# Kernel tuning notes

Measured on AMD Instinct MI355X. Metric: run time of the kernel, lower is better.

## Reference

```python
import jax, jax.numpy as jnp
import numpy as np
from jax import lax

KERNEL = 3
SAMPLING_RATE = 100.0
N_GRID = 201  # np.linspace(-1, 1, 201) sub-sample grid


def setup_inputs() -> dict:
    key = jax.random.key(0)
    nb, nc, nx, nt = 32, 3, 64, 4096
    xcorr = jax.random.normal(key, (nb, nc, nx, nt), dtype=jnp.float32)
    return {"xcorr": xcorr, "nlag": nt // 2}


def reference(xcorr, nlag):
    nt = xcorr.shape[-1]
    x = jnp.abs(xcorr)  # vabs=True

    # max_pool2d with (1, kernel=3), stride 1, padding (0, 1) -> SAME max over lag axis
    smax = lax.reduce_window(
        x, -jnp.inf, lax.max,
        window_dimensions=(1, 1, 1, KERNEL),
        window_strides=(1, 1, 1, 1),
        padding=[(0, 0), (0, 0), (0, 0), (KERNEL // 2, KERNEL // 2)],
    )
    keep = (smax == x).astype(x.dtype)

    # top-2 local maxima along lag axis (sorted descending, like torch.topk)
    topk_score, topk_idx = lax.top_k(x * keep, 2)
    s0 = topk_score[..., 0]
    s1 = topk_score[..., 1]
    weight = (0.1 + 3.0 * (s0 - s1)) * s0 ** 2
    i0 = topk_idx[..., 0]  # [nb, nc, nx]

    # --- sub-sample interpolation: 3-point spline == parabola through neighbors ---
    offsets = jnp.array([-1, 0, 1], dtype=i0.dtype)
    nbr_idx = jnp.clip(i0[..., None] + offsets, 0, nt - 1)      # [nb,nc,nx,3]
    y = jnp.take_along_axis(x, nbr_idx, axis=-1)                 # [nb,nc,nx,3]
    ym1, y0, yp1 = y[..., 0], y[..., 1], y[..., 2]
    a = 0.5 * (ym1 + yp1) - y0   # quadratic coeff
    b = 0.5 * (yp1 - ym1)        # linear coeff
    c = y0                       # constant

    xg = jnp.linspace(-1.0, 1.0, N_GRID, dtype=x.dtype)          # [201]
    yg = (a[..., None] * xg + b[..., None]) * xg + c[..., None]  # [nb,nc,nx,201]
    ii = jnp.argmax(yg, axis=-1)                                  # [nb,nc,nx]
    sub_shift = xg[ii]
    topk_idx_f = i0.astype(x.dtype) + sub_shift
    topk_score0 = jnp.take_along_axis(yg, ii[..., None], axis=-1)[..., 0]

    # pick the channel with the largest weight
    idx = jnp.argmax(weight, axis=1, keepdims=True)               # [nb,1,nx]
    max_cc = jnp.take_along_axis(topk_score0, idx, axis=1)
    w = jnp.take_along_axis(weight, idx, axis=1)
    shift_idx = jnp.take_along_axis(topk_idx_f, idx, axis=1) - jnp.asarray(nlag, x.dtype)
    shift_t = shift_idx / SAMPLING_RATE

    # stacked: [cc_max, cc_weight, cc_dt, cc_shift], each [nb,1,nx]
    return jnp.stack([max_cc, w, shift_t, shift_idx], axis=0)
```

## Files before the change

### kernel.cpp

```cpp
#include <hip/hip_runtime.h>
#include <math.h>

#define NB 32
#define NC 3
#define NX 64
#define NT 4096
#define NGRID 201

__device__ __forceinline__ bool better(float va, int ia, float vb, int ib) {
    return (va > vb) || (va == vb && ia < ib);
}

__global__ __launch_bounds__(256) void detect_peaks_kernel(
    const float* __restrict__ xcorr,
    const int*   __restrict__ nlag_p,
    float* __restrict__ out)
{
    __shared__ float rv0[4], rv1[4];
    __shared__ int   ri0[4], ri1[4];

    const int bid  = blockIdx.x;
    const int b    = bid / NX;
    const int x    = bid % NX;
    const int tid  = threadIdx.x;
    const int lane = tid & 63;
    const int wid  = tid >> 6;

    float best_w = -INFINITY, best_s = 0.0f, best_f = 0.0f;

    for (int c = 0; c < NC; ++c) {
        const float* __restrict__ xr =
            xcorr + ((size_t)((b * NC + c) * NX) + x) * NT;

        float v0 = -1.0f, v1 = -1.0f;
        int   i0 = 0x7fffffff, i1 = 0x7fffffff;

        #pragma unroll
        for (int k = 0; k < 4; ++k) {
            const int t4 = (k * 256 + tid) * 4;
            const float4 v = *reinterpret_cast<const float4*>(xr + t4);
            const float a0 = fabsf(v.x), a1 = fabsf(v.y);
            const float a2 = fabsf(v.z), a3 = fabsf(v.w);

            float lm = __shfl_up(a3, 1);
            float rm = __shfl_down(a0, 1);
            if (lane == 0)  lm = (t4 > 0)      ? fabsf(xr[t4 - 1]) : -INFINITY;
            if (lane == 63) rm = (t4 + 4 < NT) ? fabsf(xr[t4 + 4]) : -INFINITY;

            const float c0 = (a0 >= lm && a0 >= a1) ? a0 : 0.0f;
            const float c1 = (a1 >= a0 && a1 >= a2) ? a1 : 0.0f;
            const float c2 = (a2 >= a1 && a2 >= a3) ? a2 : 0.0f;
            const float c3 = (a3 >= a2 && a3 >= rm) ? a3 : 0.0f;

            if (c0 > v0)      { v1 = v0; i1 = i0; v0 = c0; i0 = t4;     }
            else if (c0 > v1) { v1 = c0; i1 = t4;                       }
            if (c1 > v0)      { v1 = v0; i1 = i0; v0 = c1; i0 = t4 + 1; }
            else if (c1 > v1) { v1 = c1; i1 = t4 + 1;                   }
            if (c2 > v0)      { v1 = v0; i1 = i0; v0 = c2; i0 = t4 + 2; }
            else if (c2 > v1) { v1 = c2; i1 = t4 + 2;                   }
            if (c3 > v0)      { v1 = v0; i1 = i0; v0 = c3; i0 = t4 + 3; }
            else if (c3 > v1) { v1 = c3; i1 = t4 + 3;                   }
        }

        #pragma unroll
        for (int off = 1; off < 64; off <<= 1) {
            const float ov0 = __shfl_xor(v0, off);
            const int   oi0 = __shfl_xor(i0, off);
            const float ov1 = __shfl_xor(v1, off);
            const int   oi1 = __shfl_xor(i1, off);
            if (better(ov0, oi0, v0, i0)) {
                float nv1; int ni1;
                if (better(v0, i0, ov1, oi1)) { nv1 = v0;  ni1 = i0;  }
                else                          { nv1 = ov1; ni1 = oi1; }
                v0 = ov0; i0 = oi0; v1 = nv1; i1 = ni1;
            } else {
                if (better(ov0, oi0, v1, i1)) { v1 = ov0; i1 = oi0; }
            }
        }

        if (lane == 0) { rv0[wid] = v0; ri0[wid] = i0; rv1[wid] = v1; ri1[wid] = i1; }
        __syncthreads();

        if (tid < 64) {
            float a0 = rv0[0], a1 = rv1[0];
            int   ai0 = ri0[0], ai1 = ri1[0];
            #pragma unroll
            for (int w = 1; w < 4; ++w) {
                const float b0 = rv0[w], b1 = rv1[w];
                const int   bi0 = ri0[w], bi1 = ri1[w];
                if (better(b0, bi0, a0, ai0)) {
                    float nv1; int ni1;
                    if (better(a0, ai0, b1, bi1)) { nv1 = a0; ni1 = ai0; }
                    else                          { nv1 = b1; ni1 = bi1; }
                    a0 = b0; ai0 = bi0; a1 = nv1; ai1 = ni1;
                } else {
                    if (better(b0, bi0, a1, ai1)) { a1 = b0; ai1 = bi0; }
                }
            }

            const float s0 = a0, s1 = a1;
            const int   p0 = ai0;
            const float weight = (0.1f + 3.0f * (s0 - s1)) * (s0 * s0);

            const int im1 = (p0 - 1 < 0) ? 0 : p0 - 1;
            const int ip1 = (p0 + 1 > NT - 1) ? NT - 1 : p0 + 1;
            const float ym1 = fabsf(xr[im1]);
            const float yc  = fabsf(xr[p0]);
            const float yp1 = fabsf(xr[ip1]);
            const float A = 0.5f * (ym1 + yp1) - yc;
            const float B = 0.5f * (yp1 - ym1);
            const float C = yc;

            float bv = -INFINITY; int bi = 0x7fffffff;
            #pragma unroll
            for (int k = 0; k < 4; ++k) {
                const int gi = lane + k * 64;
                if (gi < NGRID) {
                    const float xg = 0.01f * (float)(gi - 100);
                    const float yg = (A * xg + B) * xg + C;
                    if (yg > bv) { bv = yg; bi = gi; }
                }
            }
            #pragma unroll
            for (int off = 1; off < 64; off <<= 1) {
                const float ov = __shfl_xor(bv, off);
                const int   oi = __shfl_xor(bi, off);
                if (ov > bv || (ov == bv && oi < bi)) { bv = ov; bi = oi; }
            }

            if (weight > best_w) {
                best_w = weight;
                best_s = bv;
                best_f = (float)p0 + 0.01f * (float)(bi - 100);
            }
        }
        __syncthreads();
    }

    if (tid == 0) {
        const float nlagf = (float)(*nlag_p);
        const int n = NB * NX;
        const int o = b * NX + x;
        const float shift_idx = best_f - nlagf;
        out[0 * n + o] = best_s;
        out[1 * n + o] = best_w;
        out[2 * n + o] = shift_idx / 100.0f;
        out[3 * n + o] = shift_idx;
    }
}

extern "C" void kernel_launch(void* const* d_in, const int* in_sizes, int n_in,
                              void* d_out, int out_size, void* d_ws, size_t ws_size,
                              hipStream_t stream) {
    const float* xcorr  = (const float*)d_in[0];
    const int*   nlag_p = (const int*)d_in[1];
    float* out = (float*)d_out;

    detect_peaks_kernel<<<NB * NX, 256, 0, stream>>>(xcorr, nlag_p, out);
}
```

Baseline: 29.26 us.

## Process all channels in one pass and carry peak neighbors through reductions

```diff
diff --git a/kernel.cpp b/kernel.cpp
--- a/kernel.cpp
+++ b/kernel.cpp
@@ -16,8 +16,8 @@
     const int*   __restrict__ nlag_p,
     float* __restrict__ out)
 {
-    __shared__ float rv0[4], rv1[4];
-    __shared__ int   ri0[4], ri1[4];
+    __shared__ float sv0[NC][4], sv1[NC][4], snm[NC][4], snp[NC][4];
+    __shared__ int   si0[NC][4], si1[NC][4];
 
     const int bid  = blockIdx.x;
     const int b    = bid / NX;
@@ -26,90 +26,112 @@
     const int lane = tid & 63;
     const int wid  = tid >> 6;
 
-    float best_w = -INFINITY, best_s = 0.0f, best_f = 0.0f;
+    const float* __restrict__ xr0 =
+        xcorr + ((size_t)(b * NC) * NX + x) * NT;
 
+    float v0[NC], v1[NC], n0m[NC], n0p[NC];
+    int   i0[NC], i1[NC];
+    #pragma unroll
     for (int c = 0; c < NC; ++c) {
-        const float* __restrict__ xr =
-            xcorr + ((size_t)((b * NC + c) * NX) + x) * NT;
+        v0[c] = -1.0f; v1[c] = -1.0f;
+        i0[c] = 0x7fffffff; i1[c] = 0x7fffffff;
+        n0m[c] = 0.0f; n0p[c] = 0.0f;
+    }
 
-        float v0 = -1.0f, v1 = -1.0f;
-        int   i0 = 0x7fffffff, i1 = 0x7fffffff;
-
+    #pragma unroll
+    for (int k = 0; k < 4; ++k) {
+        const int t4 = (k * 256 + tid) * 4;
         #pragma unroll
-        for (int k = 0; k < 4; ++k) {
-            const int t4 = (k * 256 + tid) * 4;
+        for (int c = 0; c < NC; ++c) {
+            const float* __restrict__ xr = xr0 + (size_t)c * (NX * NT);
             const float4 v = *reinterpret_cast<const float4*>(xr + t4);
             const float a0 = fabsf(v.x), a1 = fabsf(v.y);
             const float a2 = fabsf(v.z), a3 = fabsf(v.w);
 
             float lm = __shfl_up(a3, 1);
             float rm = __shfl_down(a0, 1);
-            if (lane == 0)  lm = (t4 > 0)      ? fabsf(xr[t4 - 1]) : -INFINITY;
-            if (lane == 63) rm = (t4 + 4 < NT) ? fabsf(xr[t4 + 4]) : -INFINITY;
+            if (lane == 0 && t4 > 0)        lm = fabsf(xr[t4 - 1]);
+            if (lane == 63 && t4 + 4 < NT)  rm = fabsf(xr[t4 + 4]);
+            const bool has_l = (t4 > 0);
+            const bool has_r = (t4 + 4 < NT);
+            const float cmp_l = has_l ? lm : -INFINITY;
+            const float cmp_r = has_r ? rm : -INFINITY;
+            const float par_l = has_l ? lm : a0;
+            const float par_r = has_r ? rm : a3;
 
-            const float c0 = (a0 >= lm && a0 >= a1) ? a0 : 0.0f;
+            const float c0 = (a0 >= cmp_l && a0 >= a1) ? a0 : 0.0f;
             const float c1 = (a1 >= a0 && a1 >= a2) ? a1 : 0.0f;
             const float c2 = (a2 >= a1 && a2 >= a3) ? a2 : 0.0f;
-            const float c3 = (a3 >= a2 && a3 >= rm) ? a3 : 0.0f;
+            const float c3 = (a3 >= a2 && a3 >= cmp_r) ? a3 : 0.0f;
 
-            if (c0 > v0)      { v1 = v0; i1 = i0; v0 = c0; i0 = t4;     }
-            else if (c0 > v1) { v1 = c0; i1 = t4;                       }
-            if (c1 > v0)      { v1 = v0; i1 = i0; v0 = c1; i0 = t4 + 1; }
-            else if (c1 > v1) { v1 = c1; i1 = t4 + 1;                   }
-            if (c2 > v0)      { v1 = v0; i1 = i0; v0 = c2; i0 = t4 + 2; }
-            else if (c2 > v1) { v1 = c2; i1 = t4 + 2;                   }
-            if (c3 > v0)      { v1 = v0; i1 = i0; v0 = c3; i0 = t4 + 3; }
-            else if (c3 > v1) { v1 = c3; i1 = t4 + 3;                   }
+            if (c0 > v0[c])      { v1[c]=v0[c]; i1[c]=i0[c]; v0[c]=c0; i0[c]=t4;   n0m[c]=par_l; n0p[c]=a1; }
+            else if (c0 > v1[c]) { v1[c]=c0; i1[c]=t4; }
+            if (c1 > v0[c])      { v1[c]=v0[c]; i1[c]=i0[c]; v0[c]=c1; i0[c]=t4+1; n0m[c]=a0; n0p[c]=a2; }
+            else if (c1 > v1[c]) { v1[c]=c1; i1[c]=t4+1; }
+            if (c2 > v0[c])      { v1[c]=v0[c]; i1[c]=i0[c]; v0[c]=c2; i0[c]=t4+2; n0m[c]=a1; n0p[c]=a3; }
+            else if (c2 > v1[c]) { v1[c]=c2; i1[c]=t4+2; }
+            if (c3 > v0[c])      { v1[c]=v0[c]; i1[c]=i0[c]; v0[c]=c3; i0[c]=t4+3; n0m[c]=a2; n0p[c]=par_r; }
+            else if (c3 > v1[c]) { v1[c]=c3; i1[c]=t4+3; }
         }
+    }
+
+    #pragma unroll
+    for (int c = 0; c < NC; ++c) {
+        #pragma unroll
+        for (int off = 1; off < 64; off <<= 1) {
+            const float ov0 = __shfl_xor(v0[c], off);
+            const int   oi0 = __shfl_xor(i0[c], off);
+            const float ov1 = __shfl_xor(v1[c], off);
+            const int   oi1 = __shfl_xor(i1[c], off);
+            const float onm = __shfl_xor(n0m[c], off);
+            const float onp = __shfl_xor(n0p[c], off);
+            if (better(ov0, oi0, v0[c], i0[c])) {
+                float nv1; int ni1;
+                if (better(v0[c], i0[c], ov1, oi1)) { nv1 = v0[c]; ni1 = i0[c]; }
+                else                                { nv1 = ov1;   ni1 = oi1;   }
+                v0[c] = ov0; i0[c] = oi0; n0m[c] = onm; n0p[c] = onp;
+                v1[c] = nv1; i1[c] = ni1;
+            } else {
+                if (better(ov0, oi0, v1[c], i1[c])) { v1[c] = ov0; i1[c] = oi0; }
+            }
+        }
+        if (lane == 0) {
+            sv0[c][wid] = v0[c]; si0[c][wid] = i0[c];
+            sv1[c][wid] = v1[c]; si1[c][wid] = i1[c];
+            snm[c][wid] = n0m[c]; snp[c][wid] = n0p[c];
+        }
+    }
+    __syncthreads();
+
+    if (tid < 64) {
+        float best_w = -INFINITY, best_s = 0.0f, best_f = 0.0f;
 
         #pragma unroll
-        for (int off = 1; off < 64; off <<= 1) {
-            const float ov0 = __shfl_xor(v0, off);
-            const int   oi0 = __shfl_xor(i0, off);
-            const float ov1 = __shfl_xor(v1, off);
-            const int   oi1 = __shfl_xor(i1, off);
-            if (better(ov0, oi0, v0, i0)) {
-                float nv1; int ni1;
-                if (better(v0, i0, ov1, oi1)) { nv1 = v0;  ni1 = i0;  }
-                else                          { nv1 = ov1; ni1 = oi1; }
-                v0 = ov0; i0 = oi0; v1 = nv1; i1 = ni1;
-            } else {
-                if (better(ov0, oi0, v1, i1)) { v1 = ov0; i1 = oi0; }
-            }
-        }
-
-        if (lane == 0) { rv0[wid] = v0; ri0[wid] = i0; rv1[wid] = v1; ri1[wid] = i1; }
-        __syncthreads();
-
-        if (tid < 64) {
-            float a0 = rv0[0], a1 = rv1[0];
-            int   ai0 = ri0[0], ai1 = ri1[0];
+        for (int c = 0; c < NC; ++c) {
+            float m0 = sv0[c][0], m1 = sv1[c][0];
+            int  mi0 = si0[c][0], mi1 = si1[c][0];
+            float nm = snm[c][0], np = snp[c][0];
             #pragma unroll
             for (int w = 1; w < 4; ++w) {
-                const float b0 = rv0[w], b1 = rv1[w];
-                const int   bi0 = ri0[w], bi1 = ri1[w];
-                if (better(b0, bi0, a0, ai0)) {
+                const float b0 = sv0[c][w], b1 = sv1[c][w];
+                const int  bi0 = si0[c][w], bi1 = si1[c][w];
+                if (better(b0, bi0, m0, mi0)) {
                     float nv1; int ni1;
-                    if (better(a0, ai0, b1, bi1)) { nv1 = a0; ni1 = ai0; }
+                    if (better(m0, mi0, b1, bi1)) { nv1 = m0; ni1 = mi0; }
                     else                          { nv1 = b1; ni1 = bi1; }
-                    a0 = b0; ai0 = bi0; a1 = nv1; ai1 = ni1;
+                    m0 = b0; mi0 = bi0; nm = snm[c][w]; np = snp[c][w];
+                    m1 = nv1; mi1 = ni1;
                 } else {
-                    if (better(b0, bi0, a1, ai1)) { a1 = b0; ai1 = bi0; }
+                    if (better(b0, bi0, m1, mi1)) { m1 = b0; mi1 = bi0; }
                 }
             }
 
-            const float s0 = a0, s1 = a1;
-            const int   p0 = ai0;
+            const float s0 = m0, s1 = m1;
             const float weight = (0.1f + 3.0f * (s0 - s1)) * (s0 * s0);
 
-            const int im1 = (p0 - 1 < 0) ? 0 : p0 - 1;
-            const int ip1 = (p0 + 1 > NT - 1) ? NT - 1 : p0 + 1;
-            const float ym1 = fabsf(xr[im1]);
-            const float yc  = fabsf(xr[p0]);
-            const float yp1 = fabsf(xr[ip1]);
-            const float A = 0.5f * (ym1 + yp1) - yc;
-            const float B = 0.5f * (yp1 - ym1);
-            const float C = yc;
+            const float A = 0.5f * (nm + np) - s0;
+            const float B = 0.5f * (np - nm);
+            const float C = s0;
 
             float bv = -INFINITY; int bi = 0x7fffffff;
             #pragma unroll
@@ -131,21 +153,20 @@
             if (weight > best_w) {
                 best_w = weight;
                 best_s = bv;
-                best_f = (float)p0 + 0.01f * (float)(bi - 100);
+                best_f = (float)mi0 + 0.01f * (float)(bi - 100);
             }
         }
-        __syncthreads();
-    }
 
-    if (tid == 0) {
-        const float nlagf = (float)(*nlag_p);
-        const int n = NB * NX;
-        const int o = b * NX + x;
-        const float shift_idx = best_f - nlagf;
-        out[0 * n + o] = best_s;
-        out[1 * n + o] = best_w;
-        out[2 * n + o] = shift_idx / 100.0f;
-        out[3 * n + o] = shift_idx;
+        if (lane == 0) {
+            const float nlagf = (float)(*nlag_p);
+            const int n = NB * NX;
+            const int o = b * NX + x;
+            const float shift_idx = best_f - nlagf;
+            out[0 * n + o] = best_s;
+            out[1 * n + o] = best_w;
+            out[2 * n + o] = shift_idx / 100.0f;
+            out[3 * n + o] = shift_idx;
+        }
     }
 }
 
```

Measured after the change: 46.14 us. 57.7% more time.

## Prefetch all three channel rows and compute sub-sample peak analytically

Applied to the files above, without the earlier changes.

```diff
diff --git a/kernel.cpp b/kernel.cpp
--- a/kernel.cpp
+++ b/kernel.cpp
@@ -5,10 +5,109 @@
 #define NC 3
 #define NX 64
 #define NT 4096
-#define NGRID 201
-
-__device__ __forceinline__ bool better(float va, int ia, float vb, int ib) {
-    return (va > vb) || (va == vb && ia < ib);
+#define CH_STRIDE ((size_t)NX * NT)
+
+struct Quad { float4 a, b, c, d; };
+
+__device__ __forceinline__ Quad load_row(const float* __restrict__ xr, int wid, int lane) {
+    const float* base = xr + (size_t)(wid << 10) + (size_t)(lane << 2);
+    Quad q;
+    q.a = *reinterpret_cast<const float4*>(base);
+    q.b = *reinterpret_cast<const float4*>(base + 256);
+    q.c = *reinterpret_cast<const float4*>(base + 512);
+    q.d = *reinterpret_cast<const float4*>(base + 768);
+    return q;
+}
+
+__device__ __forceinline__ void proc4(float a0, float a1, float a2, float a3,
+                                      float cl, float cr, int t4,
+                                      float& v0, int& i0, float& v1)
+{
+    const float c0 = (a0 >= cl && a0 >= a1) ? a0 : 0.0f;
+    const float c1 = (a1 >= a0 && a1 >= a2) ? a1 : 0.0f;
+    const float c2 = (a2 >= a1 && a2 >= a3) ? a2 : 0.0f;
+    const float c3 = (a3 >= a2 && a3 >= cr) ? a3 : 0.0f;
+    bool g;
+    g = c0 > v0; v1 = g ? v0 : fmaxf(v1, c0); v0 = fmaxf(v0, c0); i0 = g ? t4     : i0;
+    g = c1 > v0; v1 = g ? v0 : fmaxf(v1, c1); v0 = fmaxf(v0, c1); i0 = g ? t4 + 1 : i0;
+    g = c2 > v0; v1 = g ? v0 : fmaxf(v1, c2); v0 = fmaxf(v0, c2); i0 = g ? t4 + 2 : i0;
+    g = c3 > v0; v1 = g ? v0 : fmaxf(v1, c3); v0 = fmaxf(v0, c3); i0 = g ? t4 + 3 : i0;
+}
+
+__device__ __forceinline__ void scan_row(Quad q, const float* __restrict__ xr,
+                                         int wid, int lane,
+                                         float& v0, int& i0, float& v1)
+{
+    const int base = (wid << 10) + (lane << 2);
+    v0 = -1.0f; v1 = -1.0f; i0 = 0;
+
+    const float a00 = fabsf(q.a.x), a01 = fabsf(q.a.y), a02 = fabsf(q.a.z), a03 = fabsf(q.a.w);
+    const float a10 = fabsf(q.b.x), a11 = fabsf(q.b.y), a12 = fabsf(q.b.z), a13 = fabsf(q.b.w);
+    const float a20 = fabsf(q.c.x), a21 = fabsf(q.c.y), a22 = fabsf(q.c.z), a23 = fabsf(q.c.w);
+    const float a30 = fabsf(q.d.x), a31 = fabsf(q.d.y), a32 = fabsf(q.d.z), a33 = fabsf(q.d.w);
+
+    const float lmf = fabsf(xr[(wid > 0) ? (wid << 10) - 1 : 0]);
+    const float rmf = fabsf(xr[(wid < 3) ? ((wid + 1) << 10) : NT - 1]);
+
+    float lm, rm, t;
+
+    lm = __shfl_up(a03, 1);
+    lm = (lane == 0) ? ((wid > 0) ? lmf : -INFINITY) : lm;
+    rm = __shfl_down(a00, 1);
+    t  = __shfl(a10, 0);
+    rm = (lane == 63) ? t : rm;
+    proc4(a00, a01, a02, a03, lm, rm, base, v0, i0, v1);
+
+    lm = __shfl_up(a13, 1);
+    t  = __shfl(a03, 63);
+    lm = (lane == 0) ? t : lm;
+    rm = __shfl_down(a10, 1);
+    t  = __shfl(a20, 0);
+    rm = (lane == 63) ? t : rm;
+    proc4(a10, a11, a12, a13, lm, rm, base + 256, v0, i0, v1);
+
+    lm = __shfl_up(a23, 1);
+    t  = __shfl(a13, 63);
+    lm = (lane == 0) ? t : lm;
+    rm = __shfl_down(a20, 1);
+    t  = __shfl(a30, 0);
+    rm = (lane == 63) ? t : rm;
+    proc4(a20, a21, a22, a23, lm, rm, base + 512, v0, i0, v1);
+
+    lm = __shfl_up(a33, 1);
+    t  = __shfl(a23, 63);
+    lm = (lane == 0) ? t : lm;
+    rm = __shfl_down(a30, 1);
+    rm = (lane == 63) ? ((wid < 3) ? rmf : -INFINITY) : rm;
+    proc4(a30, a31, a32, a33, lm, rm, base + 768, v0, i0, v1);
+
+    #pragma unroll
+    for (int off = 1; off < 64; off <<= 1) {
+        const float ov0 = __shfl_xor(v0, off);
+        const int   oi0 = __shfl_xor(i0, off);
+        const float ov1 = __shfl_xor(v1, off);
+        const bool big = (ov0 > v0) || (ov0 == v0 && oi0 < i0);
+        const float loser = big ? v0 : ov0;
+        v1 = fmaxf(fmaxf(v1, ov1), loser);
+        v0 = big ? ov0 : v0;
+        i0 = big ? oi0 : i0;
+    }
+}
+
+__device__ __forceinline__ void merge4(const float sv0c[4], const int si0c[4],
+                                       const float sv1c[4],
+                                       float& m0, int& mi, float& m1)
+{
+    m0 = sv0c[0]; mi = si0c[0]; m1 = sv1c[0];
+    #pragma unroll
+    for (int w = 1; w < 4; ++w) {
+        const float b0 = sv0c[w]; const int bi = si0c[w]; const float b1 = sv1c[w];
+        const bool big = (b0 > m0) || (b0 == m0 && bi < mi);
+        const float loser = big ? m0 : b0;
+        m1 = fmaxf(fmaxf(m1, b1), loser);
+        m0 = big ? b0 : m0;
+        mi = big ? bi : mi;
+    }
 }
 
 __global__ __launch_bounds__(256) void detect_peaks_kernel(
@@ -16,134 +115,91 @@
     const int*   __restrict__ nlag_p,
     float* __restrict__ out)
 {
-    __shared__ float rv0[4], rv1[4];
-    __shared__ int   ri0[4], ri1[4];
+    __shared__ float sv0[NC][4], sv1[NC][4];
+    __shared__ int   si0[NC][4];
 
     const int bid  = blockIdx.x;
-    const int b    = bid / NX;
-    const int x    = bid % NX;
+    const int b    = bid >> 6;
+    const int x    = bid & 63;
     const int tid  = threadIdx.x;
     const int lane = tid & 63;
     const int wid  = tid >> 6;
 
-    float best_w = -INFINITY, best_s = 0.0f, best_f = 0.0f;
-
-    for (int c = 0; c < NC; ++c) {
-        const float* __restrict__ xr =
-            xcorr + ((size_t)((b * NC + c) * NX) + x) * NT;
-
-        float v0 = -1.0f, v1 = -1.0f;
-        int   i0 = 0x7fffffff, i1 = 0x7fffffff;
-
-        #pragma unroll
-        for (int k = 0; k < 4; ++k) {
-            const int t4 = (k * 256 + tid) * 4;
-            const float4 v = *reinterpret_cast<const float4*>(xr + t4);
-            const float a0 = fabsf(v.x), a1 = fabsf(v.y);
-            const float a2 = fabsf(v.z), a3 = fabsf(v.w);
-
-            float lm = __shfl_up(a3, 1);
-            float rm = __shfl_down(a0, 1);
-            if (lane == 0)  lm = (t4 > 0)      ? fabsf(xr[t4 - 1]) : -INFINITY;
-            if (lane == 63) rm = (t4 + 4 < NT) ? fabsf(xr[t4 + 4]) : -INFINITY;
-
-            const float c0 = (a0 >= lm && a0 >= a1) ? a0 : 0.0f;
-            const float c1 = (a1 >= a0 && a1 >= a2) ? a1 : 0.0f;
-            const float c2 = (a2 >= a1 && a2 >= a3) ? a2 : 0.0f;
-            const float c3 = (a3 >= a2 && a3 >= rm) ? a3 : 0.0f;
-
-            if (c0 > v0)      { v1 = v0; i1 = i0; v0 = c0; i0 = t4;     }
-            else if (c0 > v1) { v1 = c0; i1 = t4;                       }
-            if (c1 > v0)      { v1 = v0; i1 = i0; v0 = c1; i0 = t4 + 1; }
-            else if (c1 > v1) { v1 = c1; i1 = t4 + 1;                   }
-            if (c2 > v0)      { v1 = v0; i1 = i0; v0 = c2; i0 = t4 + 2; }
-            else if (c2 > v1) { v1 = c2; i1 = t4 + 2;                   }
-            if (c3 > v0)      { v1 = v0; i1 = i0; v0 = c3; i0 = t4 + 3; }
-            else if (c3 > v1) { v1 = c3; i1 = t4 + 3;                   }
-        }
-
-        #pragma unroll
-        for (int off = 1; off < 64; off <<= 1) {
-            const float ov0 = __shfl_xor(v0, off);
-            const int   oi0 = __shfl_xor(i0, off);
-            const float ov1 = __shfl_xor(v1, off);
-            const int   oi1 = __shfl_xor(i1, off);
-            if (better(ov0, oi0, v0, i0)) {
-                float nv1; int ni1;
-                if (better(v0, i0, ov1, oi1)) { nv1 = v0;  ni1 = i0;  }
-                else                          { nv1 = ov1; ni1 = oi1; }
-                v0 = ov0; i0 = oi0; v1 = nv1; i1 = ni1;
-            } else {
-                if (better(ov0, oi0, v1, i1)) { v1 = ov0; i1 = oi0; }
+    const float* __restrict__ xr0 = xcorr + ((size_t)(b * NC) * NX + x) * NT;
+    const float* __restrict__ xr1 = xr0 + CH_STRIDE;
+    const float* __restrict__ xr2 = xr0 + 2 * CH_STRIDE;
+
+    Quad q0 = load_row(xr0, wid, lane);
+    Quad q1 = load_row(xr1, wid, lane);
+
+    float v0, v1; int i0;
+
+    scan_row(q0, xr0, wid, lane, v0, i0, v1);
+    Quad q2 = load_row(xr2, wid, lane);
+    if (lane == 0) { sv0[0][wid] = v0; si0[0][wid] = i0; sv1[0][wid] = v1; }
+
+    scan_row(q1, xr1, wid, lane, v0, i0, v1);
+    if (lane == 0) { sv0[1][wid] = v0; si0[1][wid] = i0; sv1[1][wid] = v1; }
+
+    scan_row(q2, xr2, wid, lane, v0, i0, v1);
+    if (lane == 0) { sv0[2][wid] = v0; si0[2][wid] = i0; sv1[2][wid] = v1; }
+
+    __syncthreads();
+
+    float m00, m01, m02, m10, m11, m12; int p0, p1, p2;
+    merge4(sv0[0], si0[0], sv1[0], m00, p0, m10);
+    merge4(sv0[1], si0[1], sv1[1], m01, p1, m11);
+    merge4(sv0[2], si0[2], sv1[2], m02, p2, m12);
+
+    const float w0 = (0.1f + 3.0f * (m00 - m10)) * (m00 * m00);
+    const float w1 = (0.1f + 3.0f * (m01 - m11)) * (m01 * m01);
+    const float w2 = (0.1f + 3.0f * (m02 - m12)) * (m02 * m02);
+
+    const bool t1 = w1 > w0;
+    float bw = t1 ? w1 : w0;
+    float bs = t1 ? m01 : m00;
+    int   bp = t1 ? p1 : p0;
+    const float* xrs = t1 ? xr1 : xr0;
+    const bool t2 = w2 > bw;
+    bw  = t2 ? w2 : bw;
+    bs  = t2 ? m02 : bs;
+    bp  = t2 ? p2 : bp;
+    xrs = t2 ? xr2 : xrs;
+
+    if (tid == 0) {
+        const float ym1 = fabsf(xrs[bp > 0 ? bp - 1 : 0]);
+        const float yp1 = fabsf(xrs[bp < NT - 1 ? bp + 1 : NT - 1]);
+        const float A = 0.5f * (ym1 + yp1) - bs;
+        const float B = 0.5f * (yp1 - ym1);
+        const float C = bs;
+
+        int gi; float bv;
+        if (A == 0.0f) {
+            gi = (B > 0.0f) ? 200 : 0;
+            const float xg = 0.01f * (float)(gi - 100);
+            bv = (A * xg + B) * xg + C;
+        } else {
+            float gv = (1.0f - 0.5f * B / A) * 100.0f;
+            gv = fminf(fmaxf(gv, 0.0f), 200.0f);
+            const int glo = (int)gv;
+            bv = -INFINITY; gi = 0;
+            #pragma unroll
+            for (int d = -1; d <= 2; ++d) {
+                int g = glo + d;
+                g = g < 0 ? 0 : (g > 200 ? 200 : g);
+                const float xg = 0.01f * (float)(g - 100);
+                const float yg = (A * xg + B) * xg + C;
+                if (yg > bv) { bv = yg; gi = g; }
             }
         }
 
-        if (lane == 0) { rv0[wid] = v0; ri0[wid] = i0; rv1[wid] = v1; ri1[wid] = i1; }
-        __syncthreads();
-
-        if (tid < 64) {
-            float a0 = rv0[0], a1 = rv1[0];
-            int   ai0 = ri0[0], ai1 = ri1[0];
-            #pragma unroll
-            for (int w = 1; w < 4; ++w) {
-                const float b0 = rv0[w], b1 = rv1[w];
-                const int   bi0 = ri0[w], bi1 = ri1[w];
-                if (better(b0, bi0, a0, ai0)) {
-                    float nv1; int ni1;
-                    if (better(a0, ai0, b1, bi1)) { nv1 = a0; ni1 = ai0; }
-                    else                          { nv1 = b1; ni1 = bi1; }
-                    a0 = b0; ai0 = bi0; a1 = nv1; ai1 = ni1;
-                } else {
-                    if (better(b0, bi0, a1, ai1)) { a1 = b0; ai1 = bi0; }
-                }
-            }
-
-            const float s0 = a0, s1 = a1;
-            const int   p0 = ai0;
-            const float weight = (0.1f + 3.0f * (s0 - s1)) * (s0 * s0);
-
-            const int im1 = (p0 - 1 < 0) ? 0 : p0 - 1;
-            const int ip1 = (p0 + 1 > NT - 1) ? NT - 1 : p0 + 1;
-            const float ym1 = fabsf(xr[im1]);
-            const float yc  = fabsf(xr[p0]);
-            const float yp1 = fabsf(xr[ip1]);
-            const float A = 0.5f * (ym1 + yp1) - yc;
-            const float B = 0.5f * (yp1 - ym1);
-            const float C = yc;
-
-            float bv = -INFINITY; int bi = 0x7fffffff;
-            #pragma unroll
-            for (int k = 0; k < 4; ++k) {
-                const int gi = lane + k * 64;
-                if (gi < NGRID) {
-                    const float xg = 0.01f * (float)(gi - 100);
-                    const float yg = (A * xg + B) * xg + C;
-                    if (yg > bv) { bv = yg; bi = gi; }
-                }
-            }
-            #pragma unroll
-            for (int off = 1; off < 64; off <<= 1) {
-                const float ov = __shfl_xor(bv, off);
-                const int   oi = __shfl_xor(bi, off);
-                if (ov > bv || (ov == bv && oi < bi)) { bv = ov; bi = oi; }
-            }
-
-            if (weight > best_w) {
-                best_w = weight;
-                best_s = bv;
-                best_f = (float)p0 + 0.01f * (float)(bi - 100);
-            }
-        }
-        __syncthreads();
-    }
-
-    if (tid == 0) {
+        const float fidx = (float)bp + 0.01f * (float)(gi - 100);
         const float nlagf = (float)(*nlag_p);
+        const float shift_idx = fidx - nlagf;
         const int n = NB * NX;
         const int o = b * NX + x;
-        const float shift_idx = best_f - nlagf;
-        out[0 * n + o] = best_s;
-        out[1 * n + o] = best_w;
+        out[0 * n + o] = bv;
+        out[1 * n + o] = bw;
         out[2 * n + o] = shift_idx / 100.0f;
         out[3 * n + o] = shift_idx;
     }
```

Result: faster. 25.08 us (-14.3%).
